# Kernel optimization log

Hardware: AMD Instinct MI355X
Metric: run time of the kernel (lower is better)

The kernel has to match this reference:

```python
import jax, jax.numpy as jnp
import numpy as np

SL = 10   # seq_len hard-coded in rearrange
H = 20    # hidden size hard-coded in nn.LSTM
I = 128   # input_size
B = 32768 # batch


def setup_inputs() -> dict:
    key = jax.random.key(0)
    ks = jax.random.split(key, 9)
    k = 1.0 / np.sqrt(H)  # PyTorch LSTM init range
    u = lambda kk, shp: jax.random.uniform(kk, shp, jnp.float32, -k, k)
    return {
        "x": jax.random.normal(ks[0], (B * SL, I), jnp.float32),
        # gate order (PyTorch): i, f, g, o stacked along first dim (4H)
        "W_ih_f": u(ks[1], (4 * H, I)),
        "W_hh_f": u(ks[2], (4 * H, H)),
        "b_ih_f": u(ks[3], (4 * H,)),
        "b_hh_f": u(ks[4], (4 * H,)),
        "W_ih_b": u(ks[5], (4 * H, I)),
        "W_hh_b": u(ks[6], (4 * H, H)),
        "b_ih_b": u(ks[7], (4 * H,)),
        "b_hh_b": u(ks[8], (4 * H,)),
    }


def _lstm_scan(xp, W_hh):
    # xp: [T, B, 4H] precomputed input projection (+biases); returns hs [T, B, H]
    Bn = xp.shape[1]
    h0 = jnp.zeros((Bn, H), xp.dtype)
    c0 = jnp.zeros((Bn, H), xp.dtype)

    def step(carry, xt):
        h, c = carry
        g = xt + h @ W_hh.T
        i, f, gg, o = jnp.split(g, 4, axis=-1)
        i = jax.nn.sigmoid(i)
        f = jax.nn.sigmoid(f)
        gg = jnp.tanh(gg)
        o = jax.nn.sigmoid(o)
        c = f * c + i * gg
        h = o * jnp.tanh(c)
        return (h, c), h

    _, hs = jax.lax.scan(step, (h0, c0), xp)
    return hs


def reference(x, W_ih_f, W_hh_f, b_ih_f, b_hh_f, W_ih_b, W_hh_b, b_ih_b, b_hh_b):
    xb = x.reshape(-1, SL, I)  # '(b sl) i -> b sl i', sl=10
    # forward direction
    xp_f = jnp.einsum('bti,gi->tbg', xb, W_ih_f) + b_ih_f + b_hh_f
    hs_f = _lstm_scan(xp_f, W_hh_f)                     # [T,B,H]
    # backward direction: process reversed sequence
    xp_b = jnp.einsum('bti,gi->tbg', xb[:, ::-1], W_ih_b) + b_ih_b + b_hh_b
    hs_b = _lstm_scan(xp_b, W_hh_b)                     # [T,B,H] (reversed time order)
    # out = lstm_out[:, -1, :] : fwd hidden at t=SL-1 is hs_f[-1];
    # bwd hidden at original t=SL-1 is the FIRST reverse step, hs_b[0].
    return jnp.concatenate([hs_f[-1], hs_b[0]], axis=-1)  # [B, 2H]
```

## Files before the change

### kernel.cpp

```cpp
#include <hip/hip_runtime.h>

#define SL 10
#define NI 128

typedef float f32x4 __attribute__((ext_vector_type(4)));
typedef unsigned int u32;
typedef u32 u32x4 __attribute__((ext_vector_type(4)));
typedef _Float16 h8 __attribute__((ext_vector_type(8)));
typedef _Float16 h4 __attribute__((ext_vector_type(4)));

__device__ __forceinline__ f32x4 MFH(h8 a, h8 b, f32x4 c){
  return __builtin_amdgcn_mfma_f32_16x16x32_f16(a, b, c, 0, 0, 0);
}
__device__ __forceinline__ float sigf(float x){ return __fdividef(1.f, 1.f + __expf(-x)); }
__device__ __forceinline__ float tanhf2(float x){ return __fdividef(2.f, 1.f + __expf(-2.f*x)) - 1.f; }

__device__ __forceinline__ h8 to_h8(float4 a, float4 b){
  h8 r;
  r[0]=(_Float16)a.x; r[1]=(_Float16)a.y; r[2]=(_Float16)a.z; r[3]=(_Float16)a.w;
  r[4]=(_Float16)b.x; r[5]=(_Float16)b.y; r[6]=(_Float16)b.z; r[7]=(_Float16)b.w;
  return r;
}

__global__ __launch_bounds__(64, 2) void bilstm_kernel(
    const float* __restrict__ x,
    const float* __restrict__ Wih_f, const float* __restrict__ Whh_f,
    const float* __restrict__ bih_f, const float* __restrict__ bhh_f,
    const float* __restrict__ Wih_b,
    const float* __restrict__ bih_b, const float* __restrict__ bhh_b,
    float* __restrict__ out)
{
  __shared__ __attribute__((aligned(16))) char XT[8192];
  __shared__ u32 HB[16*33];

  const int l  = threadIdx.x;
  const int lr = l & 15;
  const int lg = l >> 4;
  const int rh = l >> 5;
  const int kq = l & 31;
  const long b0 = (long)blockIdx.x * 16;
  const int gb = (lr&3)*20 + (lr>>2);

  for(int i=l;i<16*33;i+=64) HB[i]=0;

  const int woff = ((kq>>3)<<10) + rh*64 + (((kq>>1)&3)<<4) + ((kq&1)<<3);
  const int roff = (lr*4+lg)*16;

  const float* xsrc = x + (b0 + rh)*(long)(SL*NI) + kq*4;

  float4 buf[8];
  #pragma unroll
  for(int j=0;j<8;j++) buf[j] = *(const float4*)(xsrc + j*2*SL*NI);

  h8 WIH[20];
  #pragma unroll
  for(int p=0;p<20;p++){
    const int nt=p>>2, ks=p&3;
    const float* s = Wih_f + (gb+nt*4)*NI + ks*32 + lg*8;
    WIH[p] = to_h8(*(const float4*)s, *(const float4*)(s+4));
  }
  h8 WHH[5];
  #pragma unroll
  for(int nt=0;nt<5;nt++){
    h8 r;
    #pragma unroll
    for(int j=0;j<8;j++){
      const int k = lg*8+j;
      r[j] = (_Float16)((k<20) ? Whh_f[(gb+nt*4)*20+k] : 0.f);
    }
    WHH[nt]=r;
  }
  f32x4 biasv[5];
  #pragma unroll
  for(int nt=0;nt<5;nt++)
    #pragma unroll
    for(int ty=0;ty<4;ty++)
      biasv[nt][ty] = bih_f[ty*20+nt*4+lg] + bhh_f[ty*20+nt*4+lg];

  float cst[5]={0.f,0.f,0.f,0.f,0.f};
  h8 bx[4];
  f32x4 acc[5];

  #pragma unroll
  for(int t=0;t<SL;t++){
    const int par = (t&1)<<12;
    #pragma unroll
    for(int j=0;j<8;j++){
      float4 v = buf[j];
      h4 hv; hv[0]=(_Float16)v.x; hv[1]=(_Float16)v.y; hv[2]=(_Float16)v.z; hv[3]=(_Float16)v.w;
      *(h4*)(XT + par + woff + j*128) = hv;
    }
    if(t+1<SL){
      #pragma unroll
      for(int j=0;j<8;j++) buf[j] = *(const float4*)(xsrc + j*2*SL*NI + (t+1)*NI);
    }
    #pragma unroll
    for(int ks=0;ks<4;ks++) bx[ks] = *(const h8*)(XT + par + (ks<<10) + roff);
    u32x4 hb0, hb1;
    if(t>0){
      const u32* hp = HB + lr*33 + lg*8;
      hb0=*(const u32x4*)hp; hb1=*(const u32x4*)(hp+4);
    }
    #pragma unroll
    for(int nt=0;nt<5;nt++) acc[nt]=biasv[nt];
    #pragma unroll
    for(int ks=0;ks<4;ks++)
      #pragma unroll
      for(int nt=0;nt<5;nt++)
        acc[nt]=MFH(WIH[nt*4+ks], bx[ks], acc[nt]);
    if(t>0){
      u32x4 hh, hl;
      hh[0]=(hb0[0]>>16)|(hb0[1]&0xffff0000u);
      hh[1]=(hb0[2]>>16)|(hb0[3]&0xffff0000u);
      hh[2]=(hb1[0]>>16)|(hb1[1]&0xffff0000u);
      hh[3]=(hb1[2]>>16)|(hb1[3]&0xffff0000u);
      hl[0]=(hb0[0]&0xffffu)|(hb0[1]<<16);
      hl[1]=(hb0[2]&0xffffu)|(hb0[3]<<16);
      hl[2]=(hb1[0]&0xffffu)|(hb1[1]<<16);
      hl[3]=(hb1[2]&0xffffu)|(hb1[3]<<16);
      h8 fh=__builtin_bit_cast(h8,hh), fl=__builtin_bit_cast(h8,hl);
      #pragma unroll
      for(int nt=0;nt<5;nt++){
        acc[nt]=MFH(WHH[nt], fh, acc[nt]);
        acc[nt]=MFH(WHH[nt], fl, acc[nt]);
      }
    }
    #pragma unroll
    for(int nt=0;nt<5;nt++){
      float ig=sigf(acc[nt][0]);
      float fg=sigf(acc[nt][1]);
      float gg=tanhf2(acc[nt][2]);
      float og=sigf(acc[nt][3]);
      cst[nt]=fg*cst[nt]+ig*gg;
      float hv=og*tanhf2(cst[nt]);
      if(t==SL-1){
        out[(b0+lr)*40 + nt*4+lg] = hv;
      } else {
        _Float16 hh16=(_Float16)hv;
        _Float16 hl16=(_Float16)(hv-(float)hh16);
        HB[lr*33 + nt*4+lg] = ((u32)__builtin_bit_cast(unsigned short,hh16)<<16)
                              | (u32)__builtin_bit_cast(unsigned short,hl16);
      }
    }
  }

  f32x4 a2[5];
  #pragma unroll
  for(int nt=0;nt<5;nt++)
    #pragma unroll
    for(int ty=0;ty<4;ty++)
      a2[nt][ty] = bih_b[ty*20+nt*4+lg] + bhh_b[ty*20+nt*4+lg];
  #pragma unroll
  for(int ks=0;ks<4;ks++){
    #pragma unroll
    for(int nt=0;nt<5;nt++){
      const float* s = Wih_b + (gb+nt*4)*NI + ks*32 + lg*8;
      a2[nt]=MFH(to_h8(*(const float4*)s, *(const float4*)(s+4)), bx[ks], a2[nt]);
    }
  }
  #pragma unroll
  for(int nt=0;nt<5;nt++){
    float ig=sigf(a2[nt][0]);
    float gg=tanhf2(a2[nt][2]);
    float og=sigf(a2[nt][3]);
    out[(b0+lr)*40 + 20 + nt*4+lg] = og*tanhf2(ig*gg);
  }
}

extern "C" void kernel_launch(void* const* d_in, const int* in_sizes, int n_in,
                              void* d_out, int out_size, void* d_ws, size_t ws_size,
                              hipStream_t stream) {
  const float* x     = (const float*)d_in[0];
  const float* Wih_f = (const float*)d_in[1];
  const float* Whh_f = (const float*)d_in[2];
  const float* bih_f = (const float*)d_in[3];
  const float* bhh_f = (const float*)d_in[4];
  const float* Wih_b = (const float*)d_in[5];
  const float* bih_b = (const float*)d_in[7];
  const float* bhh_b = (const float*)d_in[8];
  float* out = (float*)d_out;
  bilstm_kernel<<<dim3(2048), dim3(64), 0, stream>>>(
      x, Wih_f, Whh_f, bih_f, bhh_f, Wih_b, bih_b, bhh_b, out);
}
```

Baseline: 55.21 us.

## Load two timesteps per stage with contiguous per-row reads and swizzled LDS

Result: slower. 63.06 us (+14.2%).

```diff
diff --git a/kernel.cpp b/kernel.cpp
--- a/kernel.cpp
+++ b/kernel.cpp
@@ -30,27 +30,28 @@
     const float* __restrict__ bih_b, const float* __restrict__ bhh_b,
     float* __restrict__ out)
 {
-  __shared__ __attribute__((aligned(16))) char XT[8192];
+  __shared__ __attribute__((aligned(16))) char XT[2][8192];
   __shared__ u32 HB[16*33];
 
   const int l  = threadIdx.x;
   const int lr = l & 15;
   const int lg = l >> 4;
-  const int rh = l >> 5;
-  const int kq = l & 31;
+  const int r  = l >> 2;
+  const int c  = l & 3;
   const long b0 = (long)blockIdx.x * 16;
   const int gb = (lr&3)*20 + (lr>>2);
 
   for(int i=l;i<16*33;i+=64) HB[i]=0;
 
-  const int woff = ((kq>>3)<<10) + rh*64 + (((kq>>1)&3)<<4) + ((kq&1)<<3);
-  const int roff = (lr*4+lg)*16;
+  const int wbase = r*512 + (c>>1)*256;
+  const int wkh   = (c&1)*128;
+  const int wswz  = (r&7)<<4;
+  const int rswz  = (lr&7)<<4;
 
-  const float* xsrc = x + (b0 + rh)*(long)(SL*NI) + kq*4;
-
-  float4 buf[8];
+  const float* xbase = x + (b0+r)*(long)(SL*NI) + c*64;
+  float4 buf[16];
   #pragma unroll
-  for(int j=0;j<8;j++) buf[j] = *(const float4*)(xsrc + j*2*SL*NI);
+  for(int i=0;i<16;i++) buf[i] = *(const float4*)(xbase + i*4);
 
   h8 WIH[20];
   #pragma unroll
@@ -62,84 +63,93 @@
   h8 WHH[5];
   #pragma unroll
   for(int nt=0;nt<5;nt++){
-    h8 r;
+    h8 w;
     #pragma unroll
     for(int j=0;j<8;j++){
       const int k = lg*8+j;
-      r[j] = (_Float16)((k<20) ? Whh_f[(gb+nt*4)*20+k] : 0.f);
+      w[j] = (_Float16)((k<20) ? Whh_f[(gb+nt*4)*20+k] : 0.f);
     }
-    WHH[nt]=r;
+    WHH[nt]=w;
   }
-  f32x4 biasv[5];
+  h4 bp[5];
   #pragma unroll
   for(int nt=0;nt<5;nt++)
     #pragma unroll
     for(int ty=0;ty<4;ty++)
-      biasv[nt][ty] = bih_f[ty*20+nt*4+lg] + bhh_f[ty*20+nt*4+lg];
+      bp[nt][ty] = (_Float16)(bih_f[ty*20+nt*4+lg] + bhh_f[ty*20+nt*4+lg]);
 
   float cst[5]={0.f,0.f,0.f,0.f,0.f};
   h8 bx[4];
   f32x4 acc[5];
 
   #pragma unroll
-  for(int t=0;t<SL;t++){
-    const int par = (t&1)<<12;
+  for(int p=0;p<5;p++){
+    char* const xt = XT[p&1];
     #pragma unroll
-    for(int j=0;j<8;j++){
-      float4 v = buf[j];
+    for(int i=0;i<16;i++){
+      float4 v = buf[i];
       h4 hv; hv[0]=(_Float16)v.x; hv[1]=(_Float16)v.y; hv[2]=(_Float16)v.z; hv[3]=(_Float16)v.w;
-      *(h4*)(XT + par + woff + j*128) = hv;
+      *(h4*)(xt + wbase + ((wkh + i*8) ^ wswz)) = hv;
     }
-    if(t+1<SL){
+    if(p<4){
       #pragma unroll
-      for(int j=0;j<8;j++) buf[j] = *(const float4*)(xsrc + j*2*SL*NI + (t+1)*NI);
+      for(int i=0;i<16;i++) buf[i] = *(const float4*)(xbase + (p+1)*256 + i*4);
     }
     #pragma unroll
-    for(int ks=0;ks<4;ks++) bx[ks] = *(const h8*)(XT + par + (ks<<10) + roff);
-    u32x4 hb0, hb1;
-    if(t>0){
-      const u32* hp = HB + lr*33 + lg*8;
-      hb0=*(const u32x4*)hp; hb1=*(const u32x4*)(hp+4);
-    }
-    #pragma unroll
-    for(int nt=0;nt<5;nt++) acc[nt]=biasv[nt];
-    #pragma unroll
-    for(int ks=0;ks<4;ks++)
+    for(int s=0;s<2;s++){
+      const int t = 2*p+s;
+      const char* rb = xt + lr*512 + s*256;
       #pragma unroll
-      for(int nt=0;nt<5;nt++)
-        acc[nt]=MFH(WIH[nt*4+ks], bx[ks], acc[nt]);
-    if(t>0){
-      u32x4 hh, hl;
-      hh[0]=(hb0[0]>>16)|(hb0[1]&0xffff0000u);
-      hh[1]=(hb0[2]>>16)|(hb0[3]&0xffff0000u);
-      hh[2]=(hb1[0]>>16)|(hb1[1]&0xffff0000u);
-      hh[3]=(hb1[2]>>16)|(hb1[3]&0xffff0000u);
-      hl[0]=(hb0[0]&0xffffu)|(hb0[1]<<16);
-      hl[1]=(hb0[2]&0xffffu)|(hb0[3]<<16);
-      hl[2]=(hb1[0]&0xffffu)|(hb1[1]<<16);
-      hl[3]=(hb1[2]&0xffffu)|(hb1[3]<<16);
-      h8 fh=__builtin_bit_cast(h8,hh), fl=__builtin_bit_cast(h8,hl);
+      for(int ks=0;ks<4;ks++)
+        bx[ks] = *(const h8*)(rb + ((ks*64 + lg*16) ^ rswz));
+      u32x4 hb0, hb1;
+      if(t>0){
+        const u32* hp = HB + lr*33 + lg*8;
+        hb0=*(const u32x4*)hp; hb1=*(const u32x4*)(hp+4);
+      }
       #pragma unroll
       for(int nt=0;nt<5;nt++){
-        acc[nt]=MFH(WHH[nt], fh, acc[nt]);
-        acc[nt]=MFH(WHH[nt], fl, acc[nt]);
+        acc[nt][0]=(float)bp[nt][0]; acc[nt][1]=(float)bp[nt][1];
+        acc[nt][2]=(float)bp[nt][2]; acc[nt][3]=(float)bp[nt][3];
       }
-    }
-    #pragma unroll
-    for(int nt=0;nt<5;nt++){
-      float ig=sigf(acc[nt][0]);
-      float fg=sigf(acc[nt][1]);
-      float gg=tanhf2(acc[nt][2]);
-      float og=sigf(acc[nt][3]);
-      cst[nt]=fg*cst[nt]+ig*gg;
-      float hv=og*tanhf2(cst[nt]);
-      if(t==SL-1){
-        out[(b0+lr)*40 + nt*4+lg] = hv;
-      } else {
-        _Float16 hh16=(_Float16)hv;
-        _Float16 hl16=(_Float16)(hv-(float)hh16);
-        HB[lr*33 + nt*4+lg] = ((u32)__builtin_bit_cast(unsigned short,hh16)<<16)
-                              | (u32)__builtin_bit_cast(unsigned short,hl16);
+      #pragma unroll
+      for(int ks=0;ks<4;ks++)
+        #pragma unroll
+        for(int nt=0;nt<5;nt++)
+          acc[nt]=MFH(WIH[nt*4+ks], bx[ks], acc[nt]);
+      if(t>0){
+        u32x4 hh, hl;
+        hh[0]=(hb0[0]>>16)|(hb0[1]&0xffff0000u);
+        hh[1]=(hb0[2]>>16)|(hb0[3]&0xffff0000u);
+        hh[2]=(hb1[0]>>16)|(hb1[1]&0xffff0000u);
+        hh[3]=(hb1[2]>>16)|(hb1[3]&0xffff0000u);
+        hl[0]=(hb0[0]&0xffffu)|(hb0[1]<<16);
+        hl[1]=(hb0[2]&0xffffu)|(hb0[3]<<16);
+        hl[2]=(hb1[0]&0xffffu)|(hb1[1]<<16);
+        hl[3]=(hb1[2]&0xffffu)|(hb1[3]<<16);
+        h8 fh=__builtin_bit_cast(h8,hh), fl=__builtin_bit_cast(h8,hl);
+        #pragma unroll
+        for(int nt=0;nt<5;nt++){
+          acc[nt]=MFH(WHH[nt], fh, acc[nt]);
+          acc[nt]=MFH(WHH[nt], fl, acc[nt]);
+        }
+      }
+      #pragma unroll
+      for(int nt=0;nt<5;nt++){
+        float ig=sigf(acc[nt][0]);
+        float fg=sigf(acc[nt][1]);
+        float gg=tanhf2(acc[nt][2]);
+        float og=sigf(acc[nt][3]);
+        cst[nt]=fg*cst[nt]+ig*gg;
+        float hv=og*tanhf2(cst[nt]);
+        if(t==SL-1){
+          out[(b0+lr)*40 + nt*4+lg] = hv;
+        } else {
+          _Float16 hh16=(_Float16)hv;
+          _Float16 hl16=(_Float16)(hv-(float)hh16);
+          HB[lr*33 + nt*4+lg] = ((u32)__builtin_bit_cast(unsigned short,hh16)<<16)
+                                | (u32)__builtin_bit_cast(unsigned short,hl16);
+        }
       }
     }
   }
```

## Warp-specialize x loading into triple-buffered LDS with dedicated loader waves

Applied to the files above, without the earlier changes.

New measurement: 158.3 us. +186.7%, slower.

```diff
diff --git a/kernel.cpp b/kernel.cpp
--- a/kernel.cpp
+++ b/kernel.cpp
@@ -2,6 +2,8 @@
 
 #define SL 10
 #define NI 128
+#define NCW 8
+#define NLW 2
 
 typedef float f32x4 __attribute__((ext_vector_type(4)));
 typedef unsigned int u32;
@@ -22,7 +24,7 @@
   return r;
 }
 
-__global__ __launch_bounds__(64, 2) void bilstm_kernel(
+__global__ __launch_bounds__(640, 3) void bilstm_kernel(
     const float* __restrict__ x,
     const float* __restrict__ Wih_f, const float* __restrict__ Whh_f,
     const float* __restrict__ bih_f, const float* __restrict__ bhh_f,
@@ -30,27 +32,62 @@
     const float* __restrict__ bih_b, const float* __restrict__ bhh_b,
     float* __restrict__ out)
 {
-  __shared__ __attribute__((aligned(16))) char XT[8192];
-  __shared__ u32 HB[16*33];
-
-  const int l  = threadIdx.x;
-  const int lr = l & 15;
-  const int lg = l >> 4;
-  const int rh = l >> 5;
-  const int kq = l & 31;
-  const long b0 = (long)blockIdx.x * 16;
-  const int gb = (lr&3)*20 + (lr>>2);
-
-  for(int i=l;i<16*33;i+=64) HB[i]=0;
-
-  const int woff = ((kq>>3)<<10) + rh*64 + (((kq>>1)&3)<<4) + ((kq&1)<<3);
-  const int roff = (lr*4+lg)*16;
-
-  const float* xsrc = x + (b0 + rh)*(long)(SL*NI) + kq*4;
-
-  float4 buf[8];
-  #pragma unroll
-  for(int j=0;j<8;j++) buf[j] = *(const float4*)(xsrc + j*2*SL*NI);
+  __shared__ __attribute__((aligned(16))) char XB[3][128*256];
+  __shared__ u32 HBa[NCW][16*33];
+
+  const int tid  = threadIdx.x;
+  const int ww   = tid >> 6;
+  const int lane = tid & 63;
+  const long b0  = (long)blockIdx.x * 128;
+
+  if(ww >= NCW){
+    const int w   = ww - NCW;
+    const int rr  = lane >> 5;
+    const int cc  = lane & 31;
+    const int wr0 = w*64 + rr;
+    const float* lsrc = x + (b0 + wr0)*(long)(SL*NI) + cc*4;
+
+    float4 lb[32];
+    #pragma unroll
+    for(int i=0;i<32;i++) lb[i] = *(const float4*)(lsrc + (long)2*i*SL*NI);
+    #pragma unroll
+    for(int i=0;i<32;i++){
+      float4 v = lb[i];
+      h4 hv; hv[0]=(_Float16)v.x; hv[1]=(_Float16)v.y; hv[2]=(_Float16)v.z; hv[3]=(_Float16)v.w;
+      const int r = wr0 + 2*i;
+      *(h4*)(XB[0] + r*256 + ((cc*8) ^ ((r&7)<<4))) = hv;
+    }
+    #pragma unroll
+    for(int i=0;i<32;i++) lb[i] = *(const float4*)(lsrc + NI + (long)2*i*SL*NI);
+    __syncthreads();
+    #pragma unroll
+    for(int t=0;t<SL-1;t++){
+      char* dst = XB[(t+1)%3];
+      #pragma unroll
+      for(int i=0;i<32;i++){
+        float4 v = lb[i];
+        h4 hv; hv[0]=(_Float16)v.x; hv[1]=(_Float16)v.y; hv[2]=(_Float16)v.z; hv[3]=(_Float16)v.w;
+        const int r = wr0 + 2*i;
+        *(h4*)(dst + r*256 + ((cc*8) ^ ((r&7)<<4))) = hv;
+      }
+      if(t+2<SL){
+        #pragma unroll
+        for(int i=0;i<32;i++) lb[i] = *(const float4*)(lsrc + (t+2)*NI + (long)2*i*SL*NI);
+      }
+      __syncthreads();
+    }
+    return;
+  }
+
+  const int lr  = lane & 15;
+  const int lg  = lane >> 4;
+  const int gb  = (lr&3)*20 + (lr>>2);
+  const long brow = b0 + ww*16 + lr;
+  const int rsw = (lr&7)<<4;
+  const int xoff = (ww*16 + lr)*256;
+  u32* HB = HBa[ww];
+
+  for(int i=lane;i<16*33;i+=64) HB[i]=0;
 
   h8 WIH[20];
   #pragma unroll
@@ -70,44 +107,37 @@
     }
     WHH[nt]=r;
   }
-  f32x4 biasv[5];
+  h4 bp[5];
   #pragma unroll
   for(int nt=0;nt<5;nt++)
     #pragma unroll
     for(int ty=0;ty<4;ty++)
-      biasv[nt][ty] = bih_f[ty*20+nt*4+lg] + bhh_f[ty*20+nt*4+lg];
+      bp[nt][ty] = (_Float16)(bih_f[ty*20+nt*4+lg] + bhh_f[ty*20+nt*4+lg]);
 
   float cst[5]={0.f,0.f,0.f,0.f,0.f};
-  h8 bx[4];
   f32x4 acc[5];
 
+  __syncthreads();
   #pragma unroll
   for(int t=0;t<SL;t++){
-    const int par = (t&1)<<12;
-    #pragma unroll
-    for(int j=0;j<8;j++){
-      float4 v = buf[j];
-      h4 hv; hv[0]=(_Float16)v.x; hv[1]=(_Float16)v.y; hv[2]=(_Float16)v.z; hv[3]=(_Float16)v.w;
-      *(h4*)(XT + par + woff + j*128) = hv;
-    }
-    if(t+1<SL){
-      #pragma unroll
-      for(int j=0;j<8;j++) buf[j] = *(const float4*)(xsrc + j*2*SL*NI + (t+1)*NI);
-    }
-    #pragma unroll
-    for(int ks=0;ks<4;ks++) bx[ks] = *(const h8*)(XT + par + (ks<<10) + roff);
+    const char* rb = XB[t%3] + xoff;
     u32x4 hb0, hb1;
     if(t>0){
       const u32* hp = HB + lr*33 + lg*8;
       hb0=*(const u32x4*)hp; hb1=*(const u32x4*)(hp+4);
     }
     #pragma unroll
-    for(int nt=0;nt<5;nt++) acc[nt]=biasv[nt];
-    #pragma unroll
-    for(int ks=0;ks<4;ks++)
+    for(int nt=0;nt<5;nt++){
+      acc[nt][0]=(float)bp[nt][0]; acc[nt][1]=(float)bp[nt][1];
+      acc[nt][2]=(float)bp[nt][2]; acc[nt][3]=(float)bp[nt][3];
+    }
+    #pragma unroll
+    for(int ks=0;ks<4;ks++){
+      h8 bx = *(const h8*)(rb + ((ks*64 + lg*16) ^ rsw));
       #pragma unroll
       for(int nt=0;nt<5;nt++)
-        acc[nt]=MFH(WIH[nt*4+ks], bx[ks], acc[nt]);
+        acc[nt]=MFH(WIH[nt*4+ks], bx, acc[nt]);
+    }
     if(t>0){
       u32x4 hh, hl;
       hh[0]=(hb0[0]>>16)|(hb0[1]&0xffff0000u);
@@ -134,7 +164,7 @@
       cst[nt]=fg*cst[nt]+ig*gg;
       float hv=og*tanhf2(cst[nt]);
       if(t==SL-1){
-        out[(b0+lr)*40 + nt*4+lg] = hv;
+        out[brow*40 + nt*4+lg] = hv;
       } else {
         _Float16 hh16=(_Float16)hv;
         _Float16 hl16=(_Float16)(hv-(float)hh16);
@@ -142,8 +172,10 @@
                               | (u32)__builtin_bit_cast(unsigned short,hl16);
       }
     }
-  }
-
+    if(t<SL-1) __syncthreads();
+  }
+
+  const char* rb9 = XB[(SL-1)%3] + xoff;
   f32x4 a2[5];
   #pragma unroll
   for(int nt=0;nt<5;nt++)
@@ -152,10 +184,11 @@
       a2[nt][ty] = bih_b[ty*20+nt*4+lg] + bhh_b[ty*20+nt*4+lg];
   #pragma unroll
   for(int ks=0;ks<4;ks++){
+    h8 bx = *(const h8*)(rb9 + ((ks*64 + lg*16) ^ rsw));
     #pragma unroll
     for(int nt=0;nt<5;nt++){
       const float* s = Wih_b + (gb+nt*4)*NI + ks*32 + lg*8;
-      a2[nt]=MFH(to_h8(*(const float4*)s, *(const float4*)(s+4)), bx[ks], a2[nt]);
+      a2[nt]=MFH(to_h8(*(const float4*)s, *(const float4*)(s+4)), bx, a2[nt]);
     }
   }
   #pragma unroll
@@ -163,7 +196,7 @@
     float ig=sigf(a2[nt][0]);
     float gg=tanhf2(a2[nt][2]);
     float og=sigf(a2[nt][3]);
-    out[(b0+lr)*40 + 20 + nt*4+lg] = og*tanhf2(ig*gg);
+    out[brow*40 + 20 + nt*4+lg] = og*tanhf2(ig*gg);
   }
 }
 
@@ -179,6 +212,6 @@
   const float* bih_b = (const float*)d_in[7];
   const float* bhh_b = (const float*)d_in[8];
   float* out = (float*)d_out;
-  bilstm_kernel<<<dim3(2048), dim3(64), 0, stream>>>(
+  bilstm_kernel<<<dim3(256), dim3(640), 0, stream>>>(
       x, Wih_f, Whh_f, bih_f, bhh_f, Wih_b, bih_b, bhh_b, out);
 }
```

## Stage all timesteps of x into swizzled LDS before recurrence loop

Applied to the files above, without the earlier changes.

After: 94.70 us. 71.5% more time.

```diff
diff --git a/kernel.cpp b/kernel.cpp
--- a/kernel.cpp
+++ b/kernel.cpp
@@ -22,7 +22,7 @@
   return r;
 }
 
-__global__ __launch_bounds__(64, 2) void bilstm_kernel(
+__global__ __launch_bounds__(64) void bilstm_kernel(
     const float* __restrict__ x,
     const float* __restrict__ Wih_f, const float* __restrict__ Whh_f,
     const float* __restrict__ bih_f, const float* __restrict__ bhh_f,
@@ -30,8 +30,8 @@
     const float* __restrict__ bih_b, const float* __restrict__ bhh_b,
     float* __restrict__ out)
 {
-  __shared__ __attribute__((aligned(16))) char XT[8192];
-  __shared__ u32 HB[16*33];
+  __shared__ __attribute__((aligned(16))) char XS[SL*4096];
+  __shared__ u32 HB[528];
 
   const int l  = threadIdx.x;
   const int lr = l & 15;
@@ -41,16 +41,33 @@
   const long b0 = (long)blockIdx.x * 16;
   const int gb = (lr&3)*20 + (lr>>2);
 
-  for(int i=l;i<16*33;i+=64) HB[i]=0;
-
-  const int woff = ((kq>>3)<<10) + rh*64 + (((kq>>1)&3)<<4) + ((kq&1)<<3);
-  const int roff = (lr*4+lg)*16;
+  for(int i=l;i<528;i+=64) HB[i]=0;
 
   const float* xsrc = x + (b0 + rh)*(long)(SL*NI) + kq*4;
-
-  float4 buf[8];
+  const int wr   = 2*0 + rh;
+  float4 pb0[8], pb1[8];
   #pragma unroll
-  for(int j=0;j<8;j++) buf[j] = *(const float4*)(xsrc + j*2*SL*NI);
+  for(int j=0;j<8;j++) pb0[j] = *(const float4*)(xsrc + (long)2*j*SL*NI);
+  #pragma unroll
+  for(int j=0;j<8;j++) pb1[j] = *(const float4*)(xsrc + NI + (long)2*j*SL*NI);
+  #pragma unroll
+  for(int t=0;t<SL;t++){
+    #pragma unroll
+    for(int j=0;j<8;j++){
+      float4 v = (t&1) ? pb1[j] : pb0[j];
+      h4 hv; hv[0]=(_Float16)v.x; hv[1]=(_Float16)v.y; hv[2]=(_Float16)v.z; hv[3]=(_Float16)v.w;
+      const int r = 2*j + rh;
+      *(h4*)(XS + t*4096 + r*256 + ((kq*8) ^ ((r&7)<<4))) = hv;
+    }
+    if(t+2<SL){
+      #pragma unroll
+      for(int j=0;j<8;j++){
+        float4 ld = *(const float4*)(xsrc + (t+2)*NI + (long)2*j*SL*NI);
+        if(t&1) pb1[j]=ld; else pb0[j]=ld;
+      }
+    }
+  }
+  (void)wr;
 
   h8 WIH[20];
   #pragma unroll
@@ -70,39 +87,34 @@
     }
     WHH[nt]=r;
   }
-  f32x4 biasv[5];
+  h4 bp[5];
   #pragma unroll
   for(int nt=0;nt<5;nt++)
     #pragma unroll
     for(int ty=0;ty<4;ty++)
-      biasv[nt][ty] = bih_f[ty*20+nt*4+lg] + bhh_f[ty*20+nt*4+lg];
+      bp[nt][ty] = (_Float16)(bih_f[ty*20+nt*4+lg] + bhh_f[ty*20+nt*4+lg]);
 
+  const int rsw = (lr&7)<<4;
   float cst[5]={0.f,0.f,0.f,0.f,0.f};
   h8 bx[4];
   f32x4 acc[5];
 
   #pragma unroll
   for(int t=0;t<SL;t++){
-    const int par = (t&1)<<12;
+    const char* rb = XS + t*4096 + lr*256;
     #pragma unroll
-    for(int j=0;j<8;j++){
-      float4 v = buf[j];
-      h4 hv; hv[0]=(_Float16)v.x; hv[1]=(_Float16)v.y; hv[2]=(_Float16)v.z; hv[3]=(_Float16)v.w;
-      *(h4*)(XT + par + woff + j*128) = hv;
-    }
-    if(t+1<SL){
-      #pragma unroll
-      for(int j=0;j<8;j++) buf[j] = *(const float4*)(xsrc + j*2*SL*NI + (t+1)*NI);
-    }
-    #pragma unroll
-    for(int ks=0;ks<4;ks++) bx[ks] = *(const h8*)(XT + par + (ks<<10) + roff);
+    for(int ks=0;ks<4;ks++)
+      bx[ks] = *(const h8*)(rb + ((ks*64 + lg*16) ^ rsw));
     u32x4 hb0, hb1;
     if(t>0){
       const u32* hp = HB + lr*33 + lg*8;
       hb0=*(const u32x4*)hp; hb1=*(const u32x4*)(hp+4);
     }
     #pragma unroll
-    for(int nt=0;nt<5;nt++) acc[nt]=biasv[nt];
+    for(int nt=0;nt<5;nt++){
+      acc[nt][0]=(float)bp[nt][0]; acc[nt][1]=(float)bp[nt][1];
+      acc[nt][2]=(float)bp[nt][2]; acc[nt][3]=(float)bp[nt][3];
+    }
     #pragma unroll
     for(int ks=0;ks<4;ks++)
       #pragma unroll
@@ -162,8 +174,9 @@
   for(int nt=0;nt<5;nt++){
     float ig=sigf(a2[nt][0]);
     float gg=tanhf2(a2[nt][2]);
-    float og=sigf(a2[nt][3]);
-    out[(b0+lr)*40 + 20 + nt*4+lg] = og*tanhf2(ig*gg);
+    float og=tanhf2(ig*gg);
+    float ogate=sigf(a2[nt][3]);
+    out[(b0+lr)*40 + 20 + nt*4+lg] = ogate*og;
   }
 }
 
```
